# Optimization experiments

Measured on AMD Instinct MI355X. Metric: run time of the kernel, lower is better.

The kernel has to match this reference:

```python
import jax, jax.numpy as jnp
import numpy as np

N_MODEL = 1024
N_HEADS = 16
KV_HEADS = 4
HEAD_DIM = N_MODEL // N_HEADS          # 64
KV_MODEL = HEAD_DIM * KV_HEADS         # 256
GROUPS = N_HEADS // KV_HEADS           # 4
B, S = 4, 2048


def _rmsnorm(x):
    return x * jax.lax.rsqrt(jnp.mean(x * x, axis=-1, keepdims=True) + 1e-6)


def _act_quant(x):
    # 8-bit absmax per-token quantization (BitNet b1.58)
    scale = 127.0 / jnp.clip(jnp.max(jnp.abs(x), axis=-1, keepdims=True), 1e-5)
    return jnp.clip(jnp.round(x * scale), -128.0, 127.0) / scale


def _weight_quant(w):
    # ternary absmean quantization
    scale = 1.0 / jnp.clip(jnp.mean(jnp.abs(w)), 1e-5)
    return jnp.clip(jnp.round(w * scale), -1.0, 1.0) / scale


def bitlinear(x, w, b):
    xn = _rmsnorm(x)
    xq = xn + jax.lax.stop_gradient(_act_quant(xn) - xn)   # STE
    wq = w + jax.lax.stop_gradient(_weight_quant(w) - w)   # STE
    return jnp.einsum('...i,oi->...o', xq, wq) + b


def setup_inputs() -> dict:
    key = jax.random.key(0)
    ks = jax.random.split(key, 11)
    sq = 1.0 / np.sqrt(N_MODEL)
    sk = 1.0 / np.sqrt(KV_MODEL)
    return {
        'query': jax.random.normal(ks[0], (B, S, N_MODEL), jnp.float32),
        'key':   jax.random.normal(ks[1], (B, S, N_MODEL), jnp.float32),
        'value': jax.random.normal(ks[2], (B, S, N_MODEL), jnp.float32),
        'Wq': jax.random.normal(ks[3], (N_MODEL, N_MODEL), jnp.float32) * sq,
        'bq': jnp.zeros((N_MODEL,), jnp.float32),
        'Wk': jax.random.normal(ks[4], (KV_MODEL, N_MODEL), jnp.float32) * sq,
        'bk': jnp.zeros((KV_MODEL,), jnp.float32),
        'Wv': jax.random.normal(ks[5], (KV_MODEL, N_MODEL), jnp.float32) * sq,
        'bv': jnp.zeros((KV_MODEL,), jnp.float32),
        'Wo': jax.random.normal(ks[6], (N_MODEL, KV_MODEL), jnp.float32) * sk,
        'bo': jnp.zeros((N_MODEL,), jnp.float32),
    }


def reference(query, key, value, Wq, bq, Wk, bk, Wv, bv, Wo, bo):
    b = query.shape[0]
    Q = bitlinear(query, Wq, bq)   # [b, n, n_model]
    K = bitlinear(key,   Wk, bk)   # [b, s, kv_model]
    V = bitlinear(value, Wv, bv)   # [b, s, kv_model]

    # [b, h, n, d] layouts
    Q = Q.reshape(b, -1, N_HEADS, HEAD_DIM).transpose(0, 2, 1, 3)
    K = K.reshape(b, -1, KV_HEADS, HEAD_DIM).transpose(0, 2, 1, 3)
    V = V.reshape(b, -1, KV_HEADS, HEAD_DIM).transpose(0, 2, 1, 3)

    # group query heads: [b, g, kv_h, n, d]
    Qg = Q.reshape(b, KV_HEADS, GROUPS, -1, HEAD_DIM).transpose(0, 2, 1, 3, 4)
    # NOTE: faithful to the module, the einsum output has no 'g' axis,
    # so the grouped query heads are SUMMED over g.
    energy = jnp.einsum('bghnd,bhsd->bhns', Qg, K)  # [b, kv_h, n, s]

    scale = jnp.sqrt(jnp.float32(HEAD_DIM))
    attention = jax.nn.softmax(energy / scale, axis=-1)
    x = jnp.einsum('bhns,bhsd->bhnd', attention, V)  # [b, kv_h, n, d]
    x = x.transpose(0, 2, 1, 3).reshape(b, -1, KV_MODEL)
    x = bitlinear(x, Wo, bo)       # [b, n, n_model]
    return (x, attention)
```

## Files before the change

### kernel.cpp

```cpp
#include <hip/hip_runtime.h>
#include <stdint.h>

#define N_MODELC 1024
#define KV_MODELC 256
#define BATCH 4
#define SEQ 2048
#define NTOK (BATCH*SEQ)
#define NZ 4
#define SCHUNK (SEQ/NZ)

typedef __attribute__((ext_vector_type(4))) float f32x4;
typedef __attribute__((ext_vector_type(4))) int   i32x4;
typedef __attribute__((ext_vector_type(8))) short s16x8;
typedef __attribute__((ext_vector_type(4))) short s16x4;

#define LOG2E 1.4426950408889634f
#define PSHIFT 32.0f

__device__ __forceinline__ unsigned short f2bf(float f){
  unsigned u = __builtin_bit_cast(unsigned, f);
  u = (u + 0x7FFFu + ((u>>16)&1u)) >> 16;
  return (unsigned short)u;
}
__device__ __forceinline__ float bf2f(unsigned short b){
  return __builtin_bit_cast(float, ((unsigned)b)<<16);
}

__global__ __launch_bounds__(256) void k_actquant1024(
    const float* __restrict__ xq_in, const float* __restrict__ xk_in, const float* __restrict__ xv_in,
    int8_t* __restrict__ q8q, int8_t* __restrict__ q8k, int8_t* __restrict__ q8v,
    float* __restrict__ scq, float* __restrict__ sck, float* __restrict__ scv)
{
  int row = blockIdx.x, which = blockIdx.y, t = threadIdx.x;
  const float* x = (which==0)?xq_in:(which==1)?xk_in:xv_in;
  int8_t* q8 = (which==0)?q8q:(which==1)?q8k:q8v;
  float* sc = (which==0)?scq:(which==1)?sck:scv;
  const float* xr = x + (size_t)row*N_MODELC;
  float4 v = reinterpret_cast<const float4*>(xr)[t];
  float ss = v.x*v.x + v.y*v.y + v.z*v.z + v.w*v.w;
  float am = fmaxf(fmaxf(fabsf(v.x),fabsf(v.y)), fmaxf(fabsf(v.z),fabsf(v.w)));
  #pragma unroll
  for (int m=32;m;m>>=1){ ss += __shfl_xor(ss,m,64); am = fmaxf(am, __shfl_xor(am,m,64)); }
  __shared__ float red[8];
  int wid = t>>6;
  if ((t&63)==0){ red[wid]=ss; red[4+wid]=am; }
  __syncthreads();
  ss = red[0]+red[1]+red[2]+red[3];
  am = fmaxf(fmaxf(red[4],red[5]), fmaxf(red[6],red[7]));
  float rinv = rsqrtf(ss*(1.0f/N_MODELC) + 1e-6f);
  float clipv = fmaxf(am*rinv, 1e-5f);
  float qs = 127.0f/clipv;
  float fsc = rinv*qs;
  char4 o;
  o.x = (signed char)(int)fminf(127.f, fmaxf(-128.f, rintf(v.x*fsc)));
  o.y = (signed char)(int)fminf(127.f, fmaxf(-128.f, rintf(v.y*fsc)));
  o.z = (signed char)(int)fminf(127.f, fmaxf(-128.f, rintf(v.z*fsc)));
  o.w = (signed char)(int)fminf(127.f, fmaxf(-128.f, rintf(v.w*fsc)));
  reinterpret_cast<char4*>(q8 + (size_t)row*N_MODELC)[t] = o;
  if (t==0) sc[row] = clipv*(1.0f/127.0f);
}

__global__ __launch_bounds__(64) void k_actquant256(
    const float* __restrict__ X, int8_t* __restrict__ q8, float* __restrict__ sc)
{
  int row = blockIdx.x, l = threadIdx.x;
  float4 v = reinterpret_cast<const float4*>(X + (size_t)row*KV_MODELC)[l];
  float ss = v.x*v.x + v.y*v.y + v.z*v.z + v.w*v.w;
  float am = fmaxf(fmaxf(fabsf(v.x),fabsf(v.y)), fmaxf(fabsf(v.z),fabsf(v.w)));
  #pragma unroll
  for (int m=32;m;m>>=1){ ss += __shfl_xor(ss,m,64); am = fmaxf(am, __shfl_xor(am,m,64)); }
  float rinv = rsqrtf(ss*(1.0f/KV_MODELC) + 1e-6f);
  float clipv = fmaxf(am*rinv, 1e-5f);
  float qs = 127.0f/clipv;
  float fsc = rinv*qs;
  char4 o;
  o.x = (signed char)(int)fminf(127.f, fmaxf(-128.f, rintf(v.x*fsc)));
  o.y = (signed char)(int)fminf(127.f, fmaxf(-128.f, rintf(v.y*fsc)));
  o.z = (signed char)(int)fminf(127.f, fmaxf(-128.f, rintf(v.z*fsc)));
  o.w = (signed char)(int)fminf(127.f, fmaxf(-128.f, rintf(v.w*fsc)));
  reinterpret_cast<char4*>(q8 + (size_t)row*KV_MODELC)[l] = o;
  if (l==0) sc[row] = clipv*(1.0f/127.0f);
}

__global__ __launch_bounds__(256) void k_wabs_partial(
    const float* __restrict__ Wq, const float* __restrict__ Wk,
    const float* __restrict__ Wv, const float* __restrict__ Wo, float* __restrict__ partial)
{
  int mat = blockIdx.y;
  const float* w = (mat==0)?Wq:(mat==1)?Wk:(mat==2)?Wv:Wo;
  int n = (mat==0)?(N_MODELC*N_MODELC):(KV_MODELC*N_MODELC);
  float s = 0.f;
  for (int i = blockIdx.x*256 + threadIdx.x; i < n; i += 256*256) s += fabsf(w[i]);
  #pragma unroll
  for (int m=32;m;m>>=1) s += __shfl_xor(s,m,64);
  __shared__ float red[4];
  int wid = threadIdx.x>>6;
  if ((threadIdx.x&63)==0) red[wid]=s;
  __syncthreads();
  if (threadIdx.x==0) partial[mat*256 + blockIdx.x] = red[0]+red[1]+red[2]+red[3];
}

__global__ __launch_bounds__(256) void k_wfinal(const float* __restrict__ partial, float* __restrict__ wfac)
{
  int mat = blockIdx.x, t = threadIdx.x;
  float s = partial[mat*256 + t];
  #pragma unroll
  for (int m=32;m;m>>=1) s += __shfl_xor(s,m,64);
  __shared__ float red[4];
  int wid = t>>6;
  if ((t&63)==0) red[wid]=s;
  __syncthreads();
  if (t==0){
    float tot = red[0]+red[1]+red[2]+red[3];
    float n = (mat==0)?(float)(N_MODELC*N_MODELC):(float)(KV_MODELC*N_MODELC);
    wfac[mat] = fmaxf(tot/n, 1e-5f);
  }
}

__global__ __launch_bounds__(256) void k_tern(
    const float* __restrict__ Wq, const float* __restrict__ Wk,
    const float* __restrict__ Wv, const float* __restrict__ Wo,
    const float* __restrict__ wfac,
    int8_t* __restrict__ Wqs, int8_t* __restrict__ Wkt,
    int8_t* __restrict__ Wvt, int8_t* __restrict__ Wot)
{
  int mat = blockIdx.y;
  int idx = blockIdx.x*256 + threadIdx.x;
  if (mat==0){
    float s = 1.0f/wfac[0];
    int op = idx>>10, i = idx&1023;
    int kv = op>>6, d = op&63;
    int acc = 0;
    #pragma unroll
    for (int g=0; g<4; g++){
      float w = Wq[(size_t)(kv*256 + g*64 + d)*N_MODELC + i];
      float r = fminf(1.f, fmaxf(-1.f, rintf(w*s)));
      acc += (int)r;
    }
    Wqs[idx] = (int8_t)acc;
  } else {
    const float* w = (mat==1)?Wk:(mat==2)?Wv:Wo;
    int8_t* o = (mat==1)?Wkt:(mat==2)?Wvt:Wot;
    float s = 1.0f/wfac[mat];
    float r = fminf(1.f, fmaxf(-1.f, rintf(w[idx]*s)));
    o[idx] = (int8_t)r;
  }
}

template<int MODE>
__global__ __launch_bounds__(512) void k_gemm_i8_1024(
    const int8_t* __restrict__ A, const int8_t* __restrict__ B,
    const float* __restrict__ rowscale, const float* __restrict__ wfac, int wfi,
    const float* __restrict__ bias, unsigned short* __restrict__ outp)
{
  __shared__ i32x4 redk[4][4][64];
  __shared__ unsigned short tlds[(MODE==2)?64:1][72];
  const int KDIM = 1024;
  int mb = blockIdx.x*64, nb = blockIdx.y*64;
  int w = threadIdx.x>>6, l = threadIdx.x&63, lr = l&15, lk = l>>4;
  int rw = w&3, kh = w>>2;
  const int8_t* Ap = A + (size_t)(mb + rw*16 + lr)*KDIM + kh*512 + lk*16;
  const int8_t* Bp = B + (size_t)(nb + lr)*KDIM + kh*512 + lk*16;
  i32x4 acc[4];
  #pragma unroll
  for (int f=0; f<4; f++) acc[f] = i32x4{0,0,0,0};
  #pragma unroll 4
  for (int kk=0; kk<512; kk+=64){
    i32x4 a = *reinterpret_cast<const i32x4*>(Ap + kk);
    #pragma unroll
    for (int f=0; f<4; f++){
      i32x4 b = *reinterpret_cast<const i32x4*>(Bp + (size_t)f*16*KDIM + kk);
      acc[f] = __builtin_amdgcn_mfma_i32_16x16x64_i8(a, b, acc[f], 0, 0, 0);
    }
  }
  if (kh==1){
    #pragma unroll
    for (int f=0; f<4; f++) redk[rw][f][l] = acc[f];
  }
  __syncthreads();
  if (kh==0){
    float wf = wfac[wfi];
    #pragma unroll
    for (int f=0; f<4; f++){
      acc[f] += redk[rw][f][l];
      int col = nb + f*16 + lr;
      float bval;
      if constexpr (MODE==0){
        int kv = col>>6, d = col&63;
        const float* bb = bias + kv*256 + d;
        bval = bb[0]+bb[64]+bb[128]+bb[192];
      } else {
        bval = bias[col];
      }
      #pragma unroll
      for (int r=0; r<4; r++){
        int row = mb + rw*16 + lk*4 + r;
        float val = (float)acc[f][r] * (rowscale[row]*wf) + bval;
        if constexpr (MODE==0){
          int bb2 = row>>11, s = row&2047, kvh = col>>6, d = col&63;
          outp[(((size_t)(bb2*4+kvh))*SEQ + s)*64 + d] = f2bf(0.125f*val);
        } else if constexpr (MODE==1){
          int bb2 = row>>11, s = row&2047, kvh = col>>6, d = col&63;
          outp[(((size_t)(bb2*4+kvh))*SEQ + s)*64 + d] = f2bf(val);
        } else {
          tlds[f*16+lr][rw*16 + lk*4 + r] = f2bf(val);
        }
      }
    }
  }
  if constexpr (MODE==2){
    __syncthreads();
    int u = threadIdx.x;
    int col = u>>3, part = u&7;
    int b = mb>>11, s0 = mb&2047;
    int bkv = b*4 + blockIdx.y, sT = s0>>6;
    s16x8 vv = *reinterpret_cast<const s16x8*>(&tlds[col][part*8]);
    *reinterpret_cast<s16x8*>(
        &outp[(((size_t)(bkv*32 + sT))*64 + col)*64 + part*8]) = vv;
  }
}

__global__ __launch_bounds__(256) void k_gemm_o(
    const int8_t* __restrict__ A, const int8_t* __restrict__ B,
    const float* __restrict__ rowscale, const float* __restrict__ wfac,
    const float* __restrict__ bias, float* __restrict__ outp)
{
  const int KDIM = 256;
  int mb = blockIdx.x*64, nb = blockIdx.y*64;
  int w = threadIdx.x>>6, l = threadIdx.x&63, lr = l&15, lk = l>>4;
  const int8_t* Ap = A + (size_t)(mb + w*16 + lr)*KDIM + lk*16;
  const int8_t* Bp = B + (size_t)(nb + lr)*KDIM + lk*16;
  i32x4 acc[4];
  #pragma unroll
  for (int f=0; f<4; f++) acc[f] = i32x4{0,0,0,0};
  #pragma unroll
  for (int kk=0; kk<KDIM; kk+=64){
    i32x4 a = *reinterpret_cast<const i32x4*>(Ap + kk);
    #pragma unroll
    for (int f=0; f<4; f++){
      i32x4 b = *reinterpret_cast<const i32x4*>(Bp + (size_t)f*16*KDIM + kk);
      acc[f] = __builtin_amdgcn_mfma_i32_16x16x64_i8(a, b, acc[f], 0, 0, 0);
    }
  }
  float wf = wfac[3];
  #pragma unroll
  for (int f=0; f<4; f++){
    int col = nb + f*16 + lr;
    float bval = bias[col];
    #pragma unroll
    for (int r=0; r<4; r++){
      int row = mb + w*16 + lk*4 + r;
      outp[(size_t)row*N_MODELC + col] = (float)acc[f][r]*(rowscale[row]*wf) + bval;
    }
  }
}

__global__ __launch_bounds__(128) void k_lsum(
    const unsigned short* __restrict__ Qh, const unsigned short* __restrict__ Kh,
    float* __restrict__ lpart)
{
  int bkv = blockIdx.y, z = blockIdx.z;
  int w = threadIdx.x>>6, l = threadIdx.x&63, lr = l&15, lk = l>>4;
  int rowt = blockIdx.x*32 + w*16;
  size_t tq = ((size_t)bkv*SEQ + rowt + lr)*64 + lk*8;
  s16x8 qa0 = *reinterpret_cast<const s16x8*>(Qh + tq);
  s16x8 qa1 = *reinterpret_cast<const s16x8*>(Qh + tq + 32);
  const unsigned short* kbase = Kh + (size_t)bkv*SEQ*64 + lk*8;
  float lsum[4] = {0.f,0.f,0.f,0.f};
  for (int s0=z*SCHUNK; s0<z*SCHUNK+SCHUNK; s0+=16){
    const unsigned short* kp = kbase + (size_t)(s0+lr)*64;
    s16x8 k0 = *reinterpret_cast<const s16x8*>(kp);
    s16x8 k1 = *reinterpret_cast<const s16x8*>(kp + 32);
    f32x4 acc = {0.f,0.f,0.f,0.f};
    acc = __builtin_amdgcn_mfma_f32_16x16x32_bf16(qa0, k0, acc, 0,0,0);
    acc = __builtin_amdgcn_mfma_f32_16x16x32_bf16(qa1, k1, acc, 0,0,0);
    #pragma unroll
    for (int r=0;r<4;r++)
      lsum[r] += __builtin_amdgcn_exp2f(fmaf(acc[r], LOG2E, -PSHIFT));
  }
  #pragma unroll
  for (int r=0;r<4;r++){
    #pragma unroll
    for (int mask=1; mask<16; mask<<=1)
      lsum[r] += __shfl_xor(lsum[r], mask, 64);
  }
  if (lr==0){
    #pragma unroll
    for (int r=0;r<4;r++)
      lpart[((size_t)z*16 + bkv)*SEQ + rowt + lk*4 + r] = lsum[r];
  }
}

__global__ __launch_bounds__(256) void k_linv(
    const float* __restrict__ lpart, float* __restrict__ invl)
{
  int idx = blockIdx.x*256 + threadIdx.x;
  float s = 0.f;
  #pragma unroll
  for (int z=0; z<NZ; z++) s += lpart[(size_t)z*16*SEQ + idx];
  invl[idx] = 1.0f/s;
}

__global__ __launch_bounds__(128) void k_attn_pv2(
    const unsigned short* __restrict__ Qh, const unsigned short* __restrict__ Kh,
    const unsigned short* __restrict__ Vh, const float* __restrict__ invl,
    float* __restrict__ attn, float* __restrict__ pvpart)
{
  __shared__ unsigned short plds[2][16][64];
  int bkv = blockIdx.y, z = blockIdx.z;
  int w = threadIdx.x>>6, l = threadIdx.x&63, lr = l&15, lk = l>>4;
  int rowt = blockIdx.x*32 + w*16;
  size_t tq = ((size_t)bkv*SEQ + rowt + lr)*64 + lk*8;
  s16x8 qa0 = *reinterpret_cast<const s16x8*>(Qh + tq);
  s16x8 qa1 = *reinterpret_cast<const s16x8*>(Qh + tq + 32);
  const unsigned short* kbase = Kh + (size_t)bkv*SEQ*64 + lk*8;
  const unsigned short* vbase = Vh + (size_t)bkv*32*4096 + lk*8;

  float invr[4];
  #pragma unroll
  for (int r=0;r<4;r++) invr[r] = invl[(size_t)bkv*SEQ + rowt + lk*4 + r];

  f32x4 acco[4];
  #pragma unroll
  for (int dt=0; dt<4; dt++) acco[dt] = f32x4{0.f,0.f,0.f,0.f};

  int qwl = lk*4;
  int rswl = (lr&7)<<3;
  float* arow = attn + (size_t)bkv*SEQ*SEQ + (size_t)rowt*SEQ;

  for (int st=z*SCHUNK; st<z*SCHUNK+SCHUNK; st+=64){
    #pragma unroll
    for (int sub=0; sub<4; sub++){
      int s0 = st + sub*16;
      const unsigned short* kp = kbase + (size_t)(s0+lr)*64;
      s16x8 k0 = *reinterpret_cast<const s16x8*>(kp);
      s16x8 k1 = *reinterpret_cast<const s16x8*>(kp + 32);
      f32x4 acc = {0.f,0.f,0.f,0.f};
      acc = __builtin_amdgcn_mfma_f32_16x16x32_bf16(qa0, k0, acc, 0,0,0);
      acc = __builtin_amdgcn_mfma_f32_16x16x32_bf16(qa1, k1, acc, 0,0,0);
      int slocal = sub*16 + lr;
      #pragma unroll
      for (int r=0;r<4;r++){
        float p = __builtin_amdgcn_exp2f(fmaf(acc[r], LOG2E, -PSHIFT))*invr[r];
        int sw = (slocal & 7) | ((((slocal>>3) ^ ((qwl+r)&7)))<<3);
        plds[w][qwl + r][sw] = f2bf(p);
      }
    }
    s16x8 a0 = *reinterpret_cast<const s16x8*>(&plds[w][lr][(lk<<3) ^ rswl]);
    s16x8 a1 = *reinterpret_cast<const s16x8*>(&plds[w][lr][((4+lk)<<3) ^ rswl]);
    const unsigned short* vt = vbase + (size_t)(st>>6)*4096;
    #pragma unroll
    for (int dt=0; dt<4; dt++){
      const unsigned short* vp = vt + (size_t)(dt*16+lr)*64;
      s16x8 b0 = *reinterpret_cast<const s16x8*>(vp);
      s16x8 b1 = *reinterpret_cast<const s16x8*>(vp + 32);
      acco[dt] = __builtin_amdgcn_mfma_f32_16x16x32_bf16(a0, b0, acco[dt], 0,0,0);
      acco[dt] = __builtin_amdgcn_mfma_f32_16x16x32_bf16(a1, b1, acco[dt], 0,0,0);
    }
    #pragma unroll
    for (int j=0; j<4; j++){
      int rowl = j*4 + (l>>4);
      int sseg = l & 15;
      int chunk = sseg >> 1, half = sseg & 1;
      int off = ((chunk ^ (rowl&7)) << 3) + (half<<2);
      s16x4 pb = *reinterpret_cast<const s16x4*>(&plds[w][rowl][off]);
      float4 o;
      o.x = bf2f((unsigned short)pb[0]);
      o.y = bf2f((unsigned short)pb[1]);
      o.z = bf2f((unsigned short)pb[2]);
      o.w = bf2f((unsigned short)pb[3]);
      *reinterpret_cast<float4*>(&arow[(size_t)rowl*SEQ + st + sseg*4]) = o;
    }
  }
  float* base = pvpart + (((size_t)z*16 + bkv)*128 + blockIdx.x*2 + w)*1024;
  #pragma unroll
  for (int dt=0; dt<4; dt++)
    *reinterpret_cast<f32x4*>(base + (dt*64 + l)*4) = acco[dt];
}

__global__ __launch_bounds__(256) void k_pvred(
    const float* __restrict__ pvpart, float* __restrict__ X)
{
  __shared__ float xls[16][65];
  int T = blockIdx.x;
  int wt = T & 127, bkv = T>>7;
  int b = bkv>>2, kv = bkv&3;
  int t = threadIdx.x, l = t&63, dt = t>>6, lk = l>>4, lr = l&15;
  f32x4 s = {0.f,0.f,0.f,0.f};
  #pragma unroll
  for (int z=0; z<NZ; z++){
    f32x4 v = *reinterpret_cast<const f32x4*>(
        pvpart + (((size_t)z*16 + bkv)*128 + wt)*1024 + t*4);
    s += v;
  }
  #pragma unroll
  for (int r=0; r<4; r++) xls[lk*4+r][dt*16+lr] = s[r];
  __syncthreads();
  int row = t>>4, col4 = (t&15)*4;
  float4 o;
  o.x = xls[row][col4];   o.y = xls[row][col4+1];
  o.z = xls[row][col4+2]; o.w = xls[row][col4+3];
  *reinterpret_cast<float4*>(
      &X[((size_t)(b*SEQ + wt*16 + row))*KV_MODELC + kv*64 + col4]) = o;
}

extern "C" void kernel_launch(void* const* d_in, const int* in_sizes, int n_in,
                              void* d_out, int out_size, void* d_ws, size_t ws_size,
                              hipStream_t stream)
{
  (void)in_sizes; (void)n_in; (void)out_size; (void)ws_size;
  const float* q  = (const float*)d_in[0];
  const float* k  = (const float*)d_in[1];
  const float* v  = (const float*)d_in[2];
  const float* Wq = (const float*)d_in[3];
  const float* bq = (const float*)d_in[4];
  const float* Wk = (const float*)d_in[5];
  const float* bk = (const float*)d_in[6];
  const float* Wv = (const float*)d_in[7];
  const float* bv = (const float*)d_in[8];
  const float* Wo = (const float*)d_in[9];
  const float* bo = (const float*)d_in[10];

  float* out_x = (float*)d_out;
  float* out_attn = out_x + (size_t)NTOK*N_MODELC;

  char* ws = (char*)d_ws;
  size_t off = 0;
  auto alloc = [&](size_t bytes)->void*{
    void* p = ws + off; off += (bytes + 255) & ~(size_t)255; return p;
  };
  int8_t* q8q = (int8_t*)alloc((size_t)NTOK*N_MODELC);
  int8_t* q8k = (int8_t*)alloc((size_t)NTOK*N_MODELC);
  int8_t* q8v = (int8_t*)alloc((size_t)NTOK*N_MODELC);
  int8_t* q8x = (int8_t*)alloc((size_t)NTOK*KV_MODELC);
  float* scq = (float*)alloc(NTOK*4);
  float* sck = (float*)alloc(NTOK*4);
  float* scv = (float*)alloc(NTOK*4);
  float* scx = (float*)alloc(NTOK*4);
  float* partial = (float*)alloc(4*256*4);
  float* wfac = (float*)alloc(256);
  int8_t* Wqs = (int8_t*)alloc(256*1024);
  int8_t* Wkt = (int8_t*)alloc(256*1024);
  int8_t* Wvt = (int8_t*)alloc(256*1024);
  int8_t* Wot = (int8_t*)alloc(1024*256);
  unsigned short* Qh = (unsigned short*)alloc((size_t)NTOK*KV_MODELC*2);
  unsigned short* Kh = (unsigned short*)alloc((size_t)NTOK*KV_MODELC*2);
  unsigned short* Vh = (unsigned short*)alloc((size_t)NTOK*KV_MODELC*2);
  float* X = (float*)alloc((size_t)NTOK*KV_MODELC*4);
  float* lpart = (float*)alloc((size_t)NZ*16*SEQ*4);
  float* invl  = (float*)alloc((size_t)16*SEQ*4);
  float* pvpart = (float*)alloc((size_t)NZ*16*128*1024*4);

  hipLaunchKernelGGL(k_actquant1024, dim3(NTOK,3), dim3(256), 0, stream,
                     q,k,v, q8q,q8k,q8v, scq,sck,scv);
  hipLaunchKernelGGL(k_wabs_partial, dim3(256,4), dim3(256), 0, stream, Wq,Wk,Wv,Wo, partial);
  hipLaunchKernelGGL(k_wfinal, dim3(4), dim3(256), 0, stream, partial, wfac);
  hipLaunchKernelGGL(k_tern, dim3(1024,4), dim3(256), 0, stream,
                     Wq,Wk,Wv,Wo, wfac, Wqs,Wkt,Wvt,Wot);
  hipLaunchKernelGGL((k_gemm_i8_1024<0>), dim3(128,4), dim3(512), 0, stream,
                     q8q, Wqs, scq, wfac, 0, bq, Qh);
  hipLaunchKernelGGL((k_gemm_i8_1024<1>), dim3(128,4), dim3(512), 0, stream,
                     q8k, Wkt, sck, wfac, 1, bk, Kh);
  hipLaunchKernelGGL((k_gemm_i8_1024<2>), dim3(128,4), dim3(512), 0, stream,
                     q8v, Wvt, scv, wfac, 2, bv, Vh);
  hipLaunchKernelGGL(k_lsum, dim3(64,16,NZ), dim3(128), 0, stream, Qh, Kh, lpart);
  hipLaunchKernelGGL(k_linv, dim3(16*SEQ/256), dim3(256), 0, stream, lpart, invl);
  hipLaunchKernelGGL(k_attn_pv2, dim3(64,16,NZ), dim3(128), 0, stream,
                     Qh, Kh, Vh, invl, out_attn, pvpart);
  hipLaunchKernelGGL(k_pvred, dim3(2048), dim3(256), 0, stream, pvpart, X);
  hipLaunchKernelGGL(k_actquant256, dim3(NTOK), dim3(64), 0, stream, X, q8x, scx);
  hipLaunchKernelGGL(k_gemm_o, dim3(128,16), dim3(256), 0, stream,
                     q8x, Wot, scx, wfac, bo, out_x);
}
```

Baseline: 334.9 us.

## Fuse softmax row-sum into attention pass and normalize with a separate expand kernel

Drops the separate QK^T/exp pass that only computed softmax denominators. The main attention kernel now computes unnormalized probabilities, gets the row sums with an MFMA against a ones vector, and writes packed bf16 probabilities into the front half of each attention row. A new kernel then expands these in place, back to front, into normalized fp32. The P·V partial results are normalized later in the reduction kernel. This removes a full recomputation of QK^T and exp, at the cost of an extra read and write pass over the large attention output.

```diff
diff --git a/kernel.cpp b/kernel.cpp
--- a/kernel.cpp
+++ b/kernel.cpp
@@ -255,56 +255,10 @@
   }
 }
 
-__global__ __launch_bounds__(128) void k_lsum(
-    const unsigned short* __restrict__ Qh, const unsigned short* __restrict__ Kh,
-    float* __restrict__ lpart)
-{
-  int bkv = blockIdx.y, z = blockIdx.z;
-  int w = threadIdx.x>>6, l = threadIdx.x&63, lr = l&15, lk = l>>4;
-  int rowt = blockIdx.x*32 + w*16;
-  size_t tq = ((size_t)bkv*SEQ + rowt + lr)*64 + lk*8;
-  s16x8 qa0 = *reinterpret_cast<const s16x8*>(Qh + tq);
-  s16x8 qa1 = *reinterpret_cast<const s16x8*>(Qh + tq + 32);
-  const unsigned short* kbase = Kh + (size_t)bkv*SEQ*64 + lk*8;
-  float lsum[4] = {0.f,0.f,0.f,0.f};
-  for (int s0=z*SCHUNK; s0<z*SCHUNK+SCHUNK; s0+=16){
-    const unsigned short* kp = kbase + (size_t)(s0+lr)*64;
-    s16x8 k0 = *reinterpret_cast<const s16x8*>(kp);
-    s16x8 k1 = *reinterpret_cast<const s16x8*>(kp + 32);
-    f32x4 acc = {0.f,0.f,0.f,0.f};
-    acc = __builtin_amdgcn_mfma_f32_16x16x32_bf16(qa0, k0, acc, 0,0,0);
-    acc = __builtin_amdgcn_mfma_f32_16x16x32_bf16(qa1, k1, acc, 0,0,0);
-    #pragma unroll
-    for (int r=0;r<4;r++)
-      lsum[r] += __builtin_amdgcn_exp2f(fmaf(acc[r], LOG2E, -PSHIFT));
-  }
-  #pragma unroll
-  for (int r=0;r<4;r++){
-    #pragma unroll
-    for (int mask=1; mask<16; mask<<=1)
-      lsum[r] += __shfl_xor(lsum[r], mask, 64);
-  }
-  if (lr==0){
-    #pragma unroll
-    for (int r=0;r<4;r++)
-      lpart[((size_t)z*16 + bkv)*SEQ + rowt + lk*4 + r] = lsum[r];
-  }
-}
-
-__global__ __launch_bounds__(256) void k_linv(
-    const float* __restrict__ lpart, float* __restrict__ invl)
-{
-  int idx = blockIdx.x*256 + threadIdx.x;
-  float s = 0.f;
-  #pragma unroll
-  for (int z=0; z<NZ; z++) s += lpart[(size_t)z*16*SEQ + idx];
-  invl[idx] = 1.0f/s;
-}
-
 __global__ __launch_bounds__(128) void k_attn_pv2(
     const unsigned short* __restrict__ Qh, const unsigned short* __restrict__ Kh,
-    const unsigned short* __restrict__ Vh, const float* __restrict__ invl,
-    float* __restrict__ attn, float* __restrict__ pvpart)
+    const unsigned short* __restrict__ Vh,
+    float* __restrict__ attn, float* __restrict__ lpart, float* __restrict__ pvpart)
 {
   __shared__ unsigned short plds[2][16][64];
   int bkv = blockIdx.y, z = blockIdx.z;
@@ -316,17 +270,18 @@
   const unsigned short* kbase = Kh + (size_t)bkv*SEQ*64 + lk*8;
   const unsigned short* vbase = Vh + (size_t)bkv*32*4096 + lk*8;
 
-  float invr[4];
-  #pragma unroll
-  for (int r=0;r<4;r++) invr[r] = invl[(size_t)bkv*SEQ + rowt + lk*4 + r];
+  s16x8 ones;
+  #pragma unroll
+  for (int i=0;i<8;i++) ones[i] = (short)0x3F80;
 
   f32x4 acco[4];
   #pragma unroll
   for (int dt=0; dt<4; dt++) acco[dt] = f32x4{0.f,0.f,0.f,0.f};
+  f32x4 accl = {0.f,0.f,0.f,0.f};
 
   int qwl = lk*4;
   int rswl = (lr&7)<<3;
-  float* arow = attn + (size_t)bkv*SEQ*SEQ + (size_t)rowt*SEQ;
+  unsigned* arow32 = (unsigned*)(attn + (size_t)bkv*SEQ*SEQ + (size_t)rowt*SEQ);
 
   for (int st=z*SCHUNK; st<z*SCHUNK+SCHUNK; st+=64){
     #pragma unroll
@@ -341,13 +296,15 @@
       int slocal = sub*16 + lr;
       #pragma unroll
       for (int r=0;r<4;r++){
-        float p = __builtin_amdgcn_exp2f(fmaf(acc[r], LOG2E, -PSHIFT))*invr[r];
+        float p = __builtin_amdgcn_exp2f(fmaf(acc[r], LOG2E, -PSHIFT));
         int sw = (slocal & 7) | ((((slocal>>3) ^ ((qwl+r)&7)))<<3);
         plds[w][qwl + r][sw] = f2bf(p);
       }
     }
     s16x8 a0 = *reinterpret_cast<const s16x8*>(&plds[w][lr][(lk<<3) ^ rswl]);
     s16x8 a1 = *reinterpret_cast<const s16x8*>(&plds[w][lr][((4+lk)<<3) ^ rswl]);
+    accl = __builtin_amdgcn_mfma_f32_16x16x32_bf16(a0, ones, accl, 0,0,0);
+    accl = __builtin_amdgcn_mfma_f32_16x16x32_bf16(a1, ones, accl, 0,0,0);
     const unsigned short* vt = vbase + (size_t)(st>>6)*4096;
     #pragma unroll
     for (int dt=0; dt<4; dt++){
@@ -364,13 +321,14 @@
       int chunk = sseg >> 1, half = sseg & 1;
       int off = ((chunk ^ (rowl&7)) << 3) + (half<<2);
       s16x4 pb = *reinterpret_cast<const s16x4*>(&plds[w][rowl][off]);
-      float4 o;
-      o.x = bf2f((unsigned short)pb[0]);
-      o.y = bf2f((unsigned short)pb[1]);
-      o.z = bf2f((unsigned short)pb[2]);
-      o.w = bf2f((unsigned short)pb[3]);
-      *reinterpret_cast<float4*>(&arow[(size_t)rowl*SEQ + st + sseg*4]) = o;
-    }
+      *reinterpret_cast<uint2*>(&arow32[(size_t)rowl*SEQ + (st>>1) + sseg*2]) =
+          *reinterpret_cast<const uint2*>(&pb);
+    }
+  }
+  if (lr==0){
+    #pragma unroll
+    for (int r=0;r<4;r++)
+      lpart[((size_t)z*16 + bkv)*SEQ + rowt + lk*4 + r] = accl[r];
   }
   float* base = pvpart + (((size_t)z*16 + bkv)*128 + blockIdx.x*2 + w)*1024;
   #pragma unroll
@@ -378,8 +336,36 @@
     *reinterpret_cast<f32x4*>(base + (dt*64 + l)*4) = acco[dt];
 }
 
+__global__ __launch_bounds__(256) void k_linv(
+    const float* __restrict__ lpart, float* __restrict__ invl)
+{
+  int idx = blockIdx.x*256 + threadIdx.x;
+  float s = 0.f;
+  #pragma unroll
+  for (int z=0; z<NZ; z++) s += lpart[(size_t)z*16*SEQ + idx];
+  invl[idx] = 1.0f/s;
+}
+
+__global__ __launch_bounds__(256) void k_expand(
+    float* __restrict__ attn, const float* __restrict__ invl)
+{
+  int w = threadIdx.x>>6, l = threadIdx.x&63;
+  int row = blockIdx.x*4 + w;
+  float iv = invl[row];
+  unsigned* src = (unsigned*)(attn + (size_t)row*SEQ);
+  float* dst = attn + (size_t)row*SEQ;
+  for (int win=15; win>=0; --win){
+    unsigned pv = src[win*64 + l];
+    float2 o;
+    o.x = bf2f((unsigned short)(pv & 0xFFFFu))*iv;
+    o.y = bf2f((unsigned short)(pv >> 16))*iv;
+    *reinterpret_cast<float2*>(&dst[(size_t)(win*64 + l)*2]) = o;
+  }
+}
+
 __global__ __launch_bounds__(256) void k_pvred(
-    const float* __restrict__ pvpart, float* __restrict__ X)
+    const float* __restrict__ pvpart, const float* __restrict__ invl,
+    float* __restrict__ X)
 {
   __shared__ float xls[16][65];
   int T = blockIdx.x;
@@ -393,8 +379,11 @@
         pvpart + (((size_t)z*16 + bkv)*128 + wt)*1024 + t*4);
     s += v;
   }
-  #pragma unroll
-  for (int r=0; r<4; r++) xls[lk*4+r][dt*16+lr] = s[r];
+  float iv[4];
+  #pragma unroll
+  for (int r=0; r<4; r++) iv[r] = invl[(size_t)bkv*SEQ + wt*16 + lk*4 + r];
+  #pragma unroll
+  for (int r=0; r<4; r++) xls[lk*4+r][dt*16+lr] = s[r]*iv[r];
   __syncthreads();
   int row = t>>4, col4 = (t&15)*4;
   float4 o;
@@ -463,11 +452,12 @@
                      q8k, Wkt, sck, wfac, 1, bk, Kh);
   hipLaunchKernelGGL((k_gemm_i8_1024<2>), dim3(128,4), dim3(512), 0, stream,
                      q8v, Wvt, scv, wfac, 2, bv, Vh);
-  hipLaunchKernelGGL(k_lsum, dim3(64,16,NZ), dim3(128), 0, stream, Qh, Kh, lpart);
+  hipLaunchKernelGGL(k_attn_pv2, dim3(64,16,NZ), dim3(128), 0, stream,
+                     Qh, Kh, Vh, out_attn, lpart, pvpart);
   hipLaunchKernelGGL(k_linv, dim3(16*SEQ/256), dim3(256), 0, stream, lpart, invl);
-  hipLaunchKernelGGL(k_attn_pv2, dim3(64,16,NZ), dim3(128), 0, stream,
-                     Qh, Kh, Vh, invl, out_attn, pvpart);
-  hipLaunchKernelGGL(k_pvred, dim3(2048), dim3(256), 0, stream, pvpart, X);
+  hipLaunchKernelGGL(k_expand, dim3(16*SEQ/4), dim3(256), 0, stream,
+                     out_attn, invl);
+  hipLaunchKernelGGL(k_pvred, dim3(2048), dim3(256), 0, stream, pvpart, invl, X);
   hipLaunchKernelGGL(k_actquant256, dim3(NTOK), dim3(64), 0, stream, X, q8x, scx);
   hipLaunchKernelGGL(k_gemm_o, dim3(128,16), dim3(256), 0, stream,
                      q8x, Wot, scx, wfac, bo, out_x);
```

Measured after the change: 346.6 us. 3.5% more time.
